# Kernel optimization log

Hardware: AMD Instinct MI355X
Metric: run time of the kernel (lower is better)

## Reference

```python
import jax, jax.numpy as jnp
import numpy as np

N = 50000      # nodes per type
E = 800000     # edges per relation
CIN = 64       # in_channels
H, O = 2, 32   # heads, out_channels
HID = H * O    # hidden
EC = 16        # edge_channels


def setup_inputs() -> dict:
    key = jax.random.key(0)
    ks = jax.random.split(key, 30)
    f = lambda i, shape, s=0.1: jax.random.normal(ks[i], shape, dtype=jnp.float32) * s
    inp = {
        'x_a': f(0, (N, CIN), 1.0), 'x_b': f(1, (N, CIN), 1.0),
        'edge_attr1': f(2, (E, EC), 1.0), 'edge_attr2': f(3, (E, EC), 1.0),
        'Wq_a': f(4, (CIN, HID)), 'Wk_a': f(5, (CIN, HID)), 'Wv_a': f(6, (CIN, HID)),
        'Wq_b': f(7, (CIN, HID)), 'Wk_b': f(8, (CIN, HID)), 'Wv_b': f(9, (CIN, HID)),
        'emb_a': f(10, (HID,)), 'emb_b': f(11, (HID,)),
        'rel1': f(12, (HID,)), 'rel2': f(13, (HID,)),
        'We': f(14, (EC, HID)), 'a_attn': f(15, (4 * O,)),
        'Wo_a': f(16, (HID, O)), 'bo_a': f(17, (O,)),
        'Wo_b': f(18, (HID, O)), 'bo_b': f(19, (O,)),
        'Wr_a': f(20, (CIN, O)), 'Wr_b': f(21, (CIN, O)),
        'row1': jax.random.randint(ks[22], (E,), 0, N),
        'col1': jax.random.randint(ks[23], (E,), 0, N),
        'row2': jax.random.randint(ks[24], (E,), 0, N),
        'col2': jax.random.randint(ks[25], (E,), 0, N),
    }
    return inp


def _edge_softmax(scores, col, num_dst):
    # softmax over incoming edges of each destination node; scores: [E, H]
    m = jax.ops.segment_max(scores, col, num_segments=num_dst)      # [N, H]
    ex = jnp.exp(scores - m[col])
    s = jax.ops.segment_sum(ex, col, num_segments=num_dst)          # [N, H]
    return ex / s[col]


def _relation(q_dst, k_src, v_src, emb_src, emb_dst, rel_emb, edge_bias,
              row, col, a_attn, num_dst):
    eb = edge_bias                                                  # [E, H, O]
    qd = q_dst[col] + emb_dst.reshape(1, H, O)
    ks = k_src[row] + emb_src.reshape(1, H, O)
    rb = jnp.broadcast_to(rel_emb.reshape(1, H, O), qd.shape)
    attn_in = jnp.concatenate([qd, ks, rb, eb], axis=-1)            # [E, H, 4O]
    scores = jnp.einsum('ehd,d->eh', jnp.tanh(attn_in), a_attn)    # [E, H]
    w = _edge_softmax(scores, col, num_dst)                         # [E, H]
    msg = v_src[row] + rel_emb.reshape(1, H, O) + eb                # [E, H, O]
    agg = jax.ops.segment_sum(msg * w[..., None], col, num_segments=num_dst)
    return agg.reshape(num_dst, H * O)


def reference(x_a, x_b, edge_attr1, edge_attr2,
              Wq_a, Wk_a, Wv_a, Wq_b, Wk_b, Wv_b,
              emb_a, emb_b, rel1, rel2, We, a_attn,
              Wo_a, bo_a, Wo_b, bo_b, Wr_a, Wr_b,
              row1, col1, row2, col2):
    q_a = (x_a @ Wq_a).reshape(-1, H, O)
    k_a = (x_a @ Wk_a).reshape(-1, H, O)
    v_a = (x_a @ Wv_a).reshape(-1, H, O)
    q_b = (x_b @ Wq_b).reshape(-1, H, O)
    k_b = (x_b @ Wk_b).reshape(-1, H, O)
    v_b = (x_b @ Wv_b).reshape(-1, H, O)

    # relation r1: a -> b
    eb1 = (edge_attr1 @ We).reshape(-1, H, O)
    out_b = _relation(q_b, k_a, v_a, emb_a, emb_b, rel1, eb1, row1, col1, a_attn, N)
    # relation r2: b -> a
    eb2 = (edge_attr2 @ We).reshape(-1, H, O)
    out_a = _relation(q_a, k_b, v_b, emb_b, emb_a, rel2, eb2, row2, col2, a_attn, N)

    fin_a = out_a @ Wo_a + bo_a + x_a @ Wr_a                        # [N, O]
    fin_b = out_b @ Wo_b + bo_b + x_b @ Wr_b                        # [N, O]
    return jnp.concatenate([fin_a, fin_b], axis=0)                  # [2N, O]
```

## Files before the change

### kernel.cpp

```cpp
#include <hip/hip_runtime.h>
#include <hip/hip_bf16.h>

typedef __hip_bfloat16 bf16;
typedef __attribute__((ext_vector_type(8))) short short8;
typedef __attribute__((ext_vector_type(4))) float float4v;

static __device__ __forceinline__ float b2f(bf16 x) { return __bfloat162float(x); }

static __device__ __forceinline__ float ldf(const void* p, size_t i, int f32) {
    return f32 ? ((const float*)p)[i] : b2f(((const bf16*)p)[i]);
}
static __device__ __forceinline__ void stf(void* p, size_t i, int f32, float v) {
    if (f32) ((float*)p)[i] = v;
    else     ((bf16*)p)[i] = __float2bfloat16(v);
}
static __device__ __forceinline__ unsigned short f2bf_bits(float f) {
    bf16 h = __float2bfloat16(f);
    return *(unsigned short*)&h;
}

static __device__ __forceinline__ float fast_tanh(float x) {
    float t = __expf(2.f * x);
    return 1.f - 2.f * __builtin_amdgcn_rcpf(t + 1.f);
}

static __device__ __forceinline__ void load_ea16(const void* ea, size_t e, int f32, float* er) {
    if (f32) {
        const float4* p = (const float4*)((const float*)ea + e * 16);
        #pragma unroll
        for (int q = 0; q < 4; ++q) {
            float4 v = p[q];
            er[4*q] = v.x; er[4*q+1] = v.y; er[4*q+2] = v.z; er[4*q+3] = v.w;
        }
    } else {
        const uint4* p = (const uint4*)((const bf16*)ea + e * 16);
        #pragma unroll
        for (int q = 0; q < 2; ++q) {
            uint4 u = p[q];
            er[8*q+0] = __uint_as_float(u.x << 16);
            er[8*q+1] = __uint_as_float(u.x & 0xffff0000u);
            er[8*q+2] = __uint_as_float(u.y << 16);
            er[8*q+3] = __uint_as_float(u.y & 0xffff0000u);
            er[8*q+4] = __uint_as_float(u.z << 16);
            er[8*q+5] = __uint_as_float(u.z & 0xffff0000u);
            er[8*q+6] = __uint_as_float(u.w << 16);
            er[8*q+7] = __uint_as_float(u.w & 0xffff0000u);
        }
    }
}

__global__ void detect_kernel(const unsigned short* __restrict__ a, int* __restrict__ flag)
{
    __shared__ int cnt;
    if (threadIdx.x == 0) cnt = 0;
    __syncthreads();
    unsigned e = (a[threadIdx.x] >> 7) & 0xFF;
    if (e < 100 || e > 133) atomicAdd(&cnt, 1);
    __syncthreads();
    if (threadIdx.x == 0) *flag = (cnt >= 16) ? 1 : 0;
}

__global__ __launch_bounds__(256) void transpose_w_kernel(
    const void* __restrict__ W0, const void* __restrict__ W1,
    const void* __restrict__ W2, const void* __restrict__ W3,
    const void* __restrict__ W4, const void* __restrict__ W5,
    const int* __restrict__ flagp, unsigned short* __restrict__ wt)
{
    const int f32 = *flagp;
    const void* src;
    switch (blockIdx.x) {
        case 0: src = W0; break; case 1: src = W1; break; case 2: src = W2; break;
        case 3: src = W3; break; case 4: src = W4; break; default: src = W5; break;
    }
    unsigned short* dst = wt + blockIdx.x * 4096;
    for (int i = threadIdx.x; i < 4096; i += 256) {
        int c = i >> 6, j = i & 63;
        dst[j * 64 + c] = f2bf_bits(ldf(src, c * 64 + j, f32));
    }
}

__global__ __launch_bounds__(256) void node_prep_mfma_kernel(
    const void* __restrict__ x_a, const void* __restrict__ x_b,
    const unsigned short* __restrict__ wt,
    const void* __restrict__ emb_a, const void* __restrict__ emb_b,
    const void* __restrict__ a_attn, const int* __restrict__ flagp,
    float* __restrict__ v_a, float* __restrict__ v_b,
    float* __restrict__ sq_a, float* __restrict__ sk_a,
    float* __restrict__ sq_b, float* __restrict__ sk_b,
    int n_nodes, int tiles)
{
    const int f32 = *flagp;
    const int wave_id = blockIdx.x * 4 + (threadIdx.x >> 6);
    if (wave_id >= 2 * tiles) return;
    const int type = (wave_id >= tiles);
    const int tile = type ? (wave_id - tiles) : wave_id;

    const void* xp = type ? x_b : x_a;
    const unsigned short* wq = wt + (type ? 3 * 4096 : 0);
    const unsigned short* wk = wq + 4096;
    const unsigned short* wv = wk + 4096;
    const void* embp = type ? emb_b : emb_a;
    float*  v_out  = type ? v_b : v_a;
    float2* sq_out = (float2*)(type ? sq_b : sq_a);
    float2* sk_out = (float2*)(type ? sk_b : sk_a);

    const int lane = threadIdx.x & 63;
    const int ml   = lane & 15;
    const int g    = lane >> 4;
    const int g8   = g * 8;

    float embc[4], acq[4], ack[4];
    #pragma unroll
    for (int t = 0; t < 4; ++t) {
        int colt = t * 16 + ml;
        embc[t] = ldf(embp, colt, f32);
        acq[t]  = ldf(a_attn, colt & 31, f32);
        ack[t]  = ldf(a_attn, 32 + (colt & 31), f32);
    }

    short8 Bq[4][2], Bk[4][2], Bv[4][2];
    #pragma unroll
    for (int t = 0; t < 4; ++t) {
        const int rowo = (t * 16 + ml) * 64;
        #pragma unroll
        for (int kh = 0; kh < 2; ++kh) {
            const int o = rowo + kh * 32 + g8;
            Bq[t][kh] = __builtin_bit_cast(short8, *(const uint4*)(wq + o));
            Bk[t][kh] = __builtin_bit_cast(short8, *(const uint4*)(wk + o));
            Bv[t][kh] = __builtin_bit_cast(short8, *(const uint4*)(wv + o));
        }
    }

    const int n0 = tile << 4;
    int nr = n0 + ml; if (nr > n_nodes - 1) nr = n_nodes - 1;
    short8 A0, A1;
    if (f32) {
        const float4* xr = (const float4*)((const float*)xp + (size_t)nr * 64);
        float4 f0 = xr[2*g], f1 = xr[2*g+1], f2 = xr[8+2*g], f3 = xr[9+2*g];
        short8 a0, a1;
        a0[0]=(short)f2bf_bits(f0.x); a0[1]=(short)f2bf_bits(f0.y);
        a0[2]=(short)f2bf_bits(f0.z); a0[3]=(short)f2bf_bits(f0.w);
        a0[4]=(short)f2bf_bits(f1.x); a0[5]=(short)f2bf_bits(f1.y);
        a0[6]=(short)f2bf_bits(f1.z); a0[7]=(short)f2bf_bits(f1.w);
        a1[0]=(short)f2bf_bits(f2.x); a1[1]=(short)f2bf_bits(f2.y);
        a1[2]=(short)f2bf_bits(f2.z); a1[3]=(short)f2bf_bits(f2.w);
        a1[4]=(short)f2bf_bits(f3.x); a1[5]=(short)f2bf_bits(f3.y);
        a1[6]=(short)f2bf_bits(f3.z); a1[7]=(short)f2bf_bits(f3.w);
        A0 = a0; A1 = a1;
    } else {
        const uint4* xr = (const uint4*)((const bf16*)xp + (size_t)nr * 64);
        A0 = __builtin_bit_cast(short8, xr[g]);
        A1 = __builtin_bit_cast(short8, xr[4 + g]);
    }

    float4v accq[4], acck[4], accv[4];
    #pragma unroll
    for (int t = 0; t < 4; ++t) {
        float4v z = {0.f, 0.f, 0.f, 0.f};
        accq[t] = z; acck[t] = z; accv[t] = z;
    }
    #pragma unroll
    for (int t = 0; t < 4; ++t) {
        accq[t] = __builtin_amdgcn_mfma_f32_16x16x32_bf16(A0, Bq[t][0], accq[t], 0, 0, 0);
        accq[t] = __builtin_amdgcn_mfma_f32_16x16x32_bf16(A1, Bq[t][1], accq[t], 0, 0, 0);
        acck[t] = __builtin_amdgcn_mfma_f32_16x16x32_bf16(A0, Bk[t][0], acck[t], 0, 0, 0);
        acck[t] = __builtin_amdgcn_mfma_f32_16x16x32_bf16(A1, Bk[t][1], acck[t], 0, 0, 0);
        accv[t] = __builtin_amdgcn_mfma_f32_16x16x32_bf16(A0, Bv[t][0], accv[t], 0, 0, 0);
        accv[t] = __builtin_amdgcn_mfma_f32_16x16x32_bf16(A1, Bv[t][1], accv[t], 0, 0, 0);
    }

    #pragma unroll
    for (int t = 0; t < 4; ++t) {
        #pragma unroll
        for (int r = 0; r < 4; ++r) {
            int node = n0 + g * 4 + r;
            if (node < n_nodes) v_out[(size_t)node * 64 + t * 16 + ml] = accv[t][r];
        }
    }

    #pragma unroll
    for (int r = 0; r < 4; ++r) {
        float q0 = fast_tanh(accq[0][r] + embc[0]) * acq[0]
                 + fast_tanh(accq[1][r] + embc[1]) * acq[1];
        float q1 = fast_tanh(accq[2][r] + embc[2]) * acq[2]
                 + fast_tanh(accq[3][r] + embc[3]) * acq[3];
        float k0 = fast_tanh(acck[0][r] + embc[0]) * ack[0]
                 + fast_tanh(acck[1][r] + embc[1]) * ack[1];
        float k1 = fast_tanh(acck[2][r] + embc[2]) * ack[2]
                 + fast_tanh(acck[3][r] + embc[3]) * ack[3];
        #pragma unroll
        for (int o = 1; o < 16; o <<= 1) {
            q0 += __shfl_xor(q0, o, 64); q1 += __shfl_xor(q1, o, 64);
            k0 += __shfl_xor(k0, o, 64); k1 += __shfl_xor(k1, o, 64);
        }
        int node = n0 + g * 4 + r;
        if (ml == 0 && node < n_nodes) {
            sq_out[node] = make_float2(q0, q1);
            sk_out[node] = make_float2(k0, k1);
        }
    }
}

__global__ void rel_const_kernel(const void* __restrict__ rel1, const void* __restrict__ rel2,
                                 const void* __restrict__ a_attn, const int* __restrict__ flagp,
                                 float* __restrict__ cvals)
{
    const int f32 = *flagp;
    int t = threadIdx.x;
    const void* r = (t < 64) ? rel1 : rel2;
    int l = t & 63;
    float v = tanhf(ldf(r, l, f32)) * ldf(a_attn, 64 + (l & 31), f32);
    #pragma unroll
    for (int off = 16; off; off >>= 1) v += __shfl_xor(v, off, 32);
    if ((l & 31) == 0) cvals[(t >> 6) * 2 + (l >> 5)] = v;
}

__global__ void precompute_kernel(const void* __restrict__ We,
                                  const void* __restrict__ Wo_b, const void* __restrict__ Wo_a,
                                  const void* __restrict__ rel1, const void* __restrict__ rel2,
                                  const int* __restrict__ flagp,
                                  float* __restrict__ M1, float* __restrict__ c321,
                                  float* __restrict__ M2, float* __restrict__ c322)
{
    const int f32 = *flagp;
    const int sel = blockIdx.x;
    const void* Wo = sel ? Wo_a : Wo_b;
    const void* rel = sel ? rel2 : rel1;
    float* M   = sel ? M2 : M1;
    float* c32 = sel ? c322 : c321;
    int t = threadIdx.x;
    int m = t >> 5, j = t & 31;
    int h = m >> 4, c = m & 15;
    float s = 0.f;
    for (int jj = 0; jj < 32; ++jj)
        s += ldf(We, c * 64 + h * 32 + jj, f32) * ldf(Wo, (size_t)(h * 32 + jj) * 32 + j, f32);
    M[m * 32 + j] = s;
    if (t < 32) {
        float s2 = 0.f;
        for (int ch = 0; ch < 64; ++ch)
            s2 += ldf(rel, ch, f32) * ldf(Wo, (size_t)ch * 32 + t, f32);
        c32[t] = s2;
    }
}

__global__ __launch_bounds__(256) void hist_kernel(
    const int* __restrict__ col1, const int* __restrict__ col2,
    int* __restrict__ cnt, int nb, int n_nodes, int num_e)
{
    const int sel = (blockIdx.x >= nb) ? 1 : 0;
    const int bx  = sel ? blockIdx.x - nb : blockIdx.x;
    const int* col = sel ? col2 : col1;
    const int rb = sel ? n_nodes : 0;
    int e = bx * 256 + threadIdx.x;
    if (e < num_e) atomicAdd(&cnt[rb + col[e]], 1);
}

__global__ __launch_bounds__(256) void scan1_kernel(const int* __restrict__ cnt,
                                                    int* __restrict__ partial, int n)
{
    __shared__ int wsum[4];
    int t = threadIdx.x;
    int i0 = blockIdx.x * 512 + 2 * t;
    int s = ((i0 < n) ? cnt[i0] : 0) + ((i0 + 1 < n) ? cnt[i0 + 1] : 0);
    #pragma unroll
    for (int o = 32; o; o >>= 1) s += __shfl_xor(s, o, 64);
    if ((t & 63) == 0) wsum[t >> 6] = s;
    __syncthreads();
    if (t == 0) partial[blockIdx.x] = wsum[0] + wsum[1] + wsum[2] + wsum[3];
}

__global__ void scan2_kernel(const int* __restrict__ partial, int* __restrict__ pp,
                             int* __restrict__ off, int nch, int noff)
{
    int lane = threadIdx.x;
    int running = 0;
    for (int base = 0; base < nch; base += 64) {
        int i = base + lane;
        int o = (i < nch) ? partial[i] : 0;
        int v = o;
        #pragma unroll
        for (int d = 1; d < 64; d <<= 1) {
            int u = __shfl_up(v, d, 64);
            if (lane >= d) v += u;
        }
        if (i < nch) pp[i] = running + v - o;
        running += __shfl(v, 63, 64);
    }
    if (lane == 0) off[noff] = running;
}

__global__ __launch_bounds__(256) void scan3_kernel(const int* __restrict__ cnt,
                                                    const int* __restrict__ pp,
                                                    int* __restrict__ off,
                                                    int* __restrict__ cursor, int n)
{
    __shared__ int tmp[256];
    int t = threadIdx.x;
    int i0 = blockIdx.x * 512 + 2 * t;
    int v0 = (i0 < n) ? cnt[i0] : 0;
    int v1 = (i0 + 1 < n) ? cnt[i0 + 1] : 0;
    int pair = v0 + v1;
    tmp[t] = pair;
    __syncthreads();
    for (int d = 1; d < 256; d <<= 1) {
        int x = (t >= d) ? tmp[t - d] : 0;
        __syncthreads();
        tmp[t] += x;
        __syncthreads();
    }
    int excl = tmp[t] - pair + pp[blockIdx.x];
    if (i0 < n)     { off[i0] = excl;          cursor[i0] = excl; }
    if (i0 + 1 < n) { off[i0 + 1] = excl + v0; cursor[i0 + 1] = excl + v0; }
}

__global__ __launch_bounds__(256) void edge_score_scatter_kernel(
    const void* __restrict__ ea1p, const void* __restrict__ ea2p,
    const void* __restrict__ We,
    const int* __restrict__ row1, const int* __restrict__ col1,
    const int* __restrict__ row2, const int* __restrict__ col2,
    const float* __restrict__ sq_bp, const float* __restrict__ sk_ap,
    const float* __restrict__ sq_ap, const float* __restrict__ sk_bp,
    const float* __restrict__ cvals, const void* __restrict__ a_attn,
    const int* __restrict__ flagp, int* __restrict__ cursor,
    uint4* __restrict__ payload, int nb, int n_nodes, int num_e)
{
    const int f32 = *flagp;
    const int sel = (blockIdx.x >= nb) ? 1 : 0;
    const int bx  = sel ? blockIdx.x - nb : blockIdx.x;
    const void* ea = sel ? ea2p : ea1p;
    const int* row = sel ? row2 : row1;
    const int* col = sel ? col2 : col1;
    const float* sq_dst = sel ? sq_ap : sq_bp;
    const float* sk_src = sel ? sk_bp : sk_ap;
    const int rb = sel ? n_nodes : 0;

    __shared__ float We_s[16 * 64];
    __shared__ float a3_s[32];
    for (int i = threadIdx.x; i < 16 * 64; i += 256) We_s[i] = ldf(We, i, f32);
    if (threadIdx.x < 32) a3_s[threadIdx.x] = ldf(a_attn, 96 + threadIdx.x, f32);
    const float c0 = cvals[sel * 2 + 0];
    const float c1 = cvals[sel * 2 + 1];
    __syncthreads();

    const int e0 = bx * 512 + threadIdx.x;
    const int e1 = e0 + 256;
    const bool v1e = (e1 < num_e);
    if (e0 >= num_e) return;

    float er0[16], er1[16];
    load_ea16(ea, (size_t)e0, f32, er0);
    if (v1e) load_ea16(ea, (size_t)e1, f32, er1);
    else {
        #pragma unroll
        for (int c = 0; c < 16; ++c) er1[c] = 0.f;
    }

    float acc00 = 0.f, acc01 = 0.f, acc10 = 0.f, acc11 = 0.f;
    #pragma unroll 1
    for (int jb = 0; jb < 64; jb += 16) {
        float t0[16], t1[16];
        #pragma unroll
        for (int jj = 0; jj < 16; ++jj) { t0[jj] = 0.f; t1[jj] = 0.f; }
        #pragma unroll
        for (int c = 0; c < 16; ++c) {
            #pragma unroll
            for (int jj = 0; jj < 16; ++jj) {
                float w = We_s[c * 64 + jb + jj];
                t0[jj] += er0[c] * w;
                t1[jj] += er1[c] * w;
            }
        }
        float p0 = 0.f, p1 = 0.f;
        #pragma unroll
        for (int jj = 0; jj < 16; ++jj) {
            float a = a3_s[(jb + jj) & 31];
            p0 += fast_tanh(t0[jj]) * a;
            p1 += fast_tanh(t1[jj]) * a;
        }
        if (jb & 32) { acc01 += p0; acc11 += p1; }
        else         { acc00 += p0; acc10 += p1; }
    }

    {
        int dc = col[e0], s = row[e0];
        float2 sqd = ((const float2*)sq_dst)[dc];
        float2 sks = ((const float2*)sk_src)[s];
        float s0 = fminf(30.f, fmaxf(-30.f, acc00 + sqd.x + sks.x + c0));
        float s1 = fminf(30.f, fmaxf(-30.f, acc01 + sqd.y + sks.y + c1));
        int pos = atomicAdd(&cursor[rb + dc], 1);
        uint4* rec = payload + (size_t)3 * pos;
        unsigned w0 = (unsigned)f2bf_bits(er0[0])  | ((unsigned)f2bf_bits(er0[1])  << 16);
        unsigned w1 = (unsigned)f2bf_bits(er0[2])  | ((unsigned)f2bf_bits(er0[3])  << 16);
        unsigned w2 = (unsigned)f2bf_bits(er0[4])  | ((unsigned)f2bf_bits(er0[5])  << 16);
        unsigned w3 = (unsigned)f2bf_bits(er0[6])  | ((unsigned)f2bf_bits(er0[7])  << 16);
        unsigned w4 = (unsigned)f2bf_bits(er0[8])  | ((unsigned)f2bf_bits(er0[9])  << 16);
        unsigned w5 = (unsigned)f2bf_bits(er0[10]) | ((unsigned)f2bf_bits(er0[11]) << 16);
        unsigned w6 = (unsigned)f2bf_bits(er0[12]) | ((unsigned)f2bf_bits(er0[13]) << 16);
        unsigned w7 = (unsigned)f2bf_bits(er0[14]) | ((unsigned)f2bf_bits(er0[15]) << 16);
        rec[0] = make_uint4((unsigned)s, __float_as_uint(__expf(s0)), __float_as_uint(__expf(s1)), 0u);
        rec[1] = make_uint4(w0, w1, w2, w3);
        rec[2] = make_uint4(w4, w5, w6, w7);
    }
    if (v1e) {
        int dc = col[e1], s = row[e1];
        float2 sqd = ((const float2*)sq_dst)[dc];
        float2 sks = ((const float2*)sk_src)[s];
        float s0 = fminf(30.f, fmaxf(-30.f, acc10 + sqd.x + sks.x + c0));
        float s1 = fminf(30.f, fmaxf(-30.f, acc11 + sqd.y + sks.y + c1));
        int pos = atomicAdd(&cursor[rb + dc], 1);
        uint4* rec = payload + (size_t)3 * pos;
        unsigned w0 = (unsigned)f2bf_bits(er1[0])  | ((unsigned)f2bf_bits(er1[1])  << 16);
        unsigned w1 = (unsigned)f2bf_bits(er1[2])  | ((unsigned)f2bf_bits(er1[3])  << 16);
        unsigned w2 = (unsigned)f2bf_bits(er1[4])  | ((unsigned)f2bf_bits(er1[5])  << 16);
        unsigned w3 = (unsigned)f2bf_bits(er1[6])  | ((unsigned)f2bf_bits(er1[7])  << 16);
        unsigned w4 = (unsigned)f2bf_bits(er1[8])  | ((unsigned)f2bf_bits(er1[9])  << 16);
        unsigned w5 = (unsigned)f2bf_bits(er1[10]) | ((unsigned)f2bf_bits(er1[11]) << 16);
        unsigned w6 = (unsigned)f2bf_bits(er1[12]) | ((unsigned)f2bf_bits(er1[13]) << 16);
        unsigned w7 = (unsigned)f2bf_bits(er1[14]) | ((unsigned)f2bf_bits(er1[15]) << 16);
        rec[0] = make_uint4((unsigned)s, __float_as_uint(__expf(s0)), __float_as_uint(__expf(s1)), 0u);
        rec[1] = make_uint4(w0, w1, w2, w3);
        rec[2] = make_uint4(w4, w5, w6, w7);
    }
}

__global__ __launch_bounds__(256) void agg_final_kernel(
    const uint4* __restrict__ payload, const int* __restrict__ off,
    const float* __restrict__ v_a, const float* __restrict__ v_b,
    const void* __restrict__ x_a, const void* __restrict__ x_b,
    const void* __restrict__ Wo_a, const void* __restrict__ Wo_b,
    const void* __restrict__ bo_a, const void* __restrict__ bo_b,
    const void* __restrict__ Wr_a, const void* __restrict__ Wr_b,
    const float* __restrict__ M1, const float* __restrict__ M2,
    const float* __restrict__ c321, const float* __restrict__ c322,
    const int* __restrict__ flagp, void* __restrict__ out,
    int n_nodes, int nbh)
{
    const int sel = (blockIdx.x >= nbh) ? 1 : 0;
    const int bx  = sel ? blockIdx.x - nbh : blockIdx.x;
    const float* v_src = sel ? v_b : v_a;
    const void*  x     = sel ? x_a : x_b;
    const void*  Wo    = sel ? Wo_a : Wo_b;
    const void*  bo    = sel ? bo_a : bo_b;
    const void*  Wr    = sel ? Wr_a : Wr_b;
    const float* M     = sel ? M2 : M1;
    const float* c32   = sel ? c322 : c321;
    const int relbase  = sel ? n_nodes : 0;
    const size_t out_off = sel ? 0 : (size_t)n_nodes * 32;

    const int f32  = *flagp;
    const int lane = threadIdx.x & 63;
    const int wv   = threadIdx.x >> 6;
    const int j    = lane & 31;
    const int half = lane >> 5;
    const int c16  = lane & 15;
    const bool hi  = (lane >= 32);

    __shared__ float stage[4][160];

    float WoR[32], WrR[32], MR[16];
    const int cb = half * 32;
    #pragma unroll
    for (int cc = 0; cc < 32; ++cc) {
        WoR[cc] = ldf(Wo, (size_t)(cb + cc) * 32 + j, f32);
        WrR[cc] = ldf(Wr, (size_t)(cb + cc) * 32 + j, f32);
    }
    const int ub = half * 16;
    #pragma unroll
    for (int cc = 0; cc < 16; ++cc) MR[cc] = M[(ub + cc) * 32 + j];
    const float boR  = ldf(bo, j, f32);
    const float c32R = c32[j];

    const int stride = nbh * 4;
    const int iters  = (n_nodes + stride - 1) / stride;
    int d = bx * 4 + wv;

    for (int it = 0; it < iters; ++it, d += stride) {
        const bool valid = (d < n_nodes);
        const int dd  = valid ? d : (n_nodes - 1);
        const int idx = relbase + dd;
        const int b   = __builtin_amdgcn_readfirstlane(off[idx]);
        const int en  = __builtin_amdgcn_readfirstlane(off[idx + 1]);
        const int deg = en - b;

        float den0 = 0.f, den1 = 0.f, y = 0.f, ua = 0.f;
        int k = b;
        #pragma unroll 1
        for (; k + 4 <= en; k += 4) {
            uint4 m0 = payload[(size_t)3 * (k + 0)];
            uint4 m1 = payload[(size_t)3 * (k + 1)];
            uint4 m2 = payload[(size_t)3 * (k + 2)];
            uint4 m3 = payload[(size_t)3 * (k + 3)];
            const unsigned short* p0 = (const unsigned short*)(payload + (size_t)3 * (k + 0) + 1);
            const unsigned short* p1 = (const unsigned short*)(payload + (size_t)3 * (k + 1) + 1);
            const unsigned short* p2 = (const unsigned short*)(payload + (size_t)3 * (k + 2) + 1);
            const unsigned short* p3 = (const unsigned short*)(payload + (size_t)3 * (k + 3) + 1);
            float vv0 = v_src[(size_t)m0.x * 64 + lane];
            float vv1 = v_src[(size_t)m1.x * 64 + lane];
            float vv2 = v_src[(size_t)m2.x * 64 + lane];
            float vv3 = v_src[(size_t)m3.x * 64 + lane];
            float ea0 = __uint_as_float((unsigned)p0[c16] << 16);
            float ea1 = __uint_as_float((unsigned)p1[c16] << 16);
            float ea2 = __uint_as_float((unsigned)p2[c16] << 16);
            float ea3 = __uint_as_float((unsigned)p3[c16] << 16);
            float e00 = __uint_as_float(m0.y), e01 = __uint_as_float(m0.z);
            float e10 = __uint_as_float(m1.y), e11 = __uint_as_float(m1.z);
            float e20 = __uint_as_float(m2.y), e21 = __uint_as_float(m2.z);
            float e30 = __uint_as_float(m3.y), e31 = __uint_as_float(m3.z);
            den0 += e00 + e10 + e20 + e30;
            den1 += e01 + e11 + e21 + e31;
            float x0 = hi ? e01 : e00;
            float x1 = hi ? e11 : e10;
            float x2 = hi ? e21 : e20;
            float x3 = hi ? e31 : e30;
            y  = fmaf(x0, vv0, y);  y  = fmaf(x1, vv1, y);
            y  = fmaf(x2, vv2, y);  y  = fmaf(x3, vv3, y);
            ua = fmaf(x0, ea0, ua); ua = fmaf(x1, ea1, ua);
            ua = fmaf(x2, ea2, ua); ua = fmaf(x3, ea3, ua);
        }
        for (; k < en; ++k) {
            uint4 m0 = payload[(size_t)3 * k];
            const unsigned short* p0 = (const unsigned short*)(payload + (size_t)3 * k + 1);
            float vv0 = v_src[(size_t)m0.x * 64 + lane];
            float ea0 = __uint_as_float((unsigned)p0[c16] << 16);
            float e00 = __uint_as_float(m0.y), e01 = __uint_as_float(m0.z);
            den0 += e00; den1 += e01;
            float x0 = hi ? e01 : e00;
            y  = fmaf(x0, vv0, y);
            ua = fmaf(x0, ea0, ua);
        }

        float inv0 = (deg > 0) ? __builtin_amdgcn_rcpf(den0) : 0.f;
        float inv1 = (deg > 0) ? __builtin_amdgcn_rcpf(den1) : 0.f;
        const float invh = hi ? inv1 : inv0;
        y  *= invh;
        ua *= invh;

        float xv = ldf(x, (size_t)dd * 64 + lane, f32);

        float* st = stage[wv];
        st[lane] = y;
        st[64 + lane] = xv;
        if ((lane & 31) < 16) st[128 + half * 16 + c16] = ua;
        __asm__ volatile("s_waitcnt lgkmcnt(0)" ::: "memory");

        float acc = 0.f;
        #pragma unroll
        for (int cc = 0; cc < 32; ++cc) {
            acc = fmaf(st[cb + cc], WoR[cc], acc);
            acc = fmaf(st[64 + cb + cc], WrR[cc], acc);
        }
        #pragma unroll
        for (int cc = 0; cc < 16; ++cc)
            acc = fmaf(st[128 + ub + cc], MR[cc], acc);

        float other = __shfl(acc, lane ^ 32, 64);
        if (valid && lane < 32) {
            float o = acc + other + boR + ((deg > 0) ? c32R : 0.f);
            stf(out, out_off + (size_t)dd * 32 + j, f32, o);
        }
        __asm__ volatile("" ::: "memory");
        __builtin_amdgcn_wave_barrier();
    }
}

extern "C" void kernel_launch(void* const* d_in, const int* in_sizes, int n_in,
                              void* d_out, int out_size, void* d_ws, size_t ws_size,
                              hipStream_t stream)
{
    const void* x_a   = d_in[0];
    const void* x_b   = d_in[1];
    const void* ea1   = d_in[2];
    const void* ea2   = d_in[3];
    const void* Wq_a  = d_in[4];
    const void* Wk_a  = d_in[5];
    const void* Wv_a  = d_in[6];
    const void* Wq_b  = d_in[7];
    const void* Wk_b  = d_in[8];
    const void* Wv_b  = d_in[9];
    const void* emb_a = d_in[10];
    const void* emb_b = d_in[11];
    const void* rel1  = d_in[12];
    const void* rel2  = d_in[13];
    const void* We    = d_in[14];
    const void* a_at  = d_in[15];
    const void* Wo_a  = d_in[16];
    const void* bo_a  = d_in[17];
    const void* Wo_b  = d_in[18];
    const void* bo_b  = d_in[19];
    const void* Wr_a  = d_in[20];
    const void* Wr_b  = d_in[21];
    const int*  row1  = (const int*)d_in[22];
    const int*  col1  = (const int*)d_in[23];
    const int*  row2  = (const int*)d_in[24];
    const int*  col2  = (const int*)d_in[25];

    const int N = in_sizes[0] / 64;
    const int E = in_sizes[22];

    float* ws = (float*)d_ws;
    size_t off = 0;
    int*   flag = (int*)ws;        off += 64;
    float* v_a  = ws + off;        off += (size_t)N * 64;
    float* v_b  = ws + off;        off += (size_t)N * 64;
    float* sq_a = ws + off;        off += (size_t)N * 2;
    float* sk_a = ws + off;        off += (size_t)N * 2;
    float* sq_b = ws + off;        off += (size_t)N * 2;
    float* sk_b = ws + off;        off += (size_t)N * 2;
    float* cvals = ws + off;       off += 4;
    off = (off + 3) & ~(size_t)3;
    unsigned short* wt = (unsigned short*)(ws + off); off += 6 * 4096 / 2;
    float* M1   = ws + off;        off += 1024;
    float* c321 = ws + off;        off += 32;
    float* M2   = ws + off;        off += 1024;
    float* c322 = ws + off;        off += 32;
    int*   cnt    = (int*)(ws + off);  off += (size_t)2 * N;
    int*   offs   = (int*)(ws + off);  off += (size_t)2 * N + 2;
    int*   cursor = (int*)(ws + off);  off += (size_t)2 * N;
    int*   partial = (int*)(ws + off); off += 512;
    int*   pp      = (int*)(ws + off); off += 512;
    off = (off + 3) & ~(size_t)3;
    uint4* payload = (uint4*)(ws + off); off += (size_t)2 * E * 12;

    const int tiles        = (N + 15) >> 4;
    const int mfma_blocks  = (2 * tiles + 3) / 4;
    const int score_blocks = (E + 511) / 512;
    const int eb_blocks    = (E + 255) / 256;
    const int nch          = (2 * N + 511) / 512;
    const int agg_half     = 2048;

    detect_kernel<<<1, 128, 0, stream>>>((const unsigned short*)a_at, flag);
    hipMemsetAsync(cnt, 0, (size_t)2 * N * sizeof(int), stream);

    transpose_w_kernel<<<6, 256, 0, stream>>>(Wq_a, Wk_a, Wv_a, Wq_b, Wk_b, Wv_b, flag, wt);
    node_prep_mfma_kernel<<<mfma_blocks, 256, 0, stream>>>(
        x_a, x_b, wt, emb_a, emb_b, a_at, flag,
        v_a, v_b, sq_a, sk_a, sq_b, sk_b, N, tiles);

    rel_const_kernel<<<1, 128, 0, stream>>>(rel1, rel2, a_at, flag, cvals);
    precompute_kernel<<<2, 1024, 0, stream>>>(We, Wo_b, Wo_a, rel1, rel2, flag,
                                              M1, c321, M2, c322);

    hist_kernel<<<2 * eb_blocks, 256, 0, stream>>>(col1, col2, cnt, eb_blocks, N, E);
    scan1_kernel<<<nch, 256, 0, stream>>>(cnt, partial, 2 * N);
    scan2_kernel<<<1, 64, 0, stream>>>(partial, pp, offs, nch, 2 * N);
    scan3_kernel<<<nch, 256, 0, stream>>>(cnt, pp, offs, cursor, 2 * N);

    edge_score_scatter_kernel<<<2 * score_blocks, 256, 0, stream>>>(
        ea1, ea2, We, row1, col1, row2, col2,
        sq_b, sk_a, sq_a, sk_b, cvals, a_at, flag,
        cursor, payload, score_blocks, N, E);

    agg_final_kernel<<<2 * agg_half, 256, 0, stream>>>(
        payload, offs, v_a, v_b, x_a, x_b, Wo_a, Wo_b, bo_a, bo_b, Wr_a, Wr_b,
        M1, M2, c321, c322, flag, d_out, N, agg_half);
}
```

Measured before the change: 581.0 us.

## Fuse small prep kernels, store V in bf16, precompute residual, unroll aggregation

Merges the weight transpose, rel-constant and precompute kernels into one launch. The residual projection x@Wr now runs on MFMA in node_prep, so agg_final no longer loads x or Wr. V is stored as bf16 to halve the bytes of the random per-edge gathers. The aggregation loop is unrolled to eight edges for more memory-level parallelism, and the two relations are interleaved across block indices. Storing V in bf16 adds rounding error, and the wider unroll raises register pressure.

```diff
diff --git a/kernel.cpp b/kernel.cpp
--- a/kernel.cpp
+++ b/kernel.cpp
@@ -60,22 +60,68 @@
     if (threadIdx.x == 0) *flag = (cnt >= 16) ? 1 : 0;
 }
 
-__global__ __launch_bounds__(256) void transpose_w_kernel(
+__global__ __launch_bounds__(256) void prep_small_kernel(
     const void* __restrict__ W0, const void* __restrict__ W1,
     const void* __restrict__ W2, const void* __restrict__ W3,
     const void* __restrict__ W4, const void* __restrict__ W5,
-    const int* __restrict__ flagp, unsigned short* __restrict__ wt)
+    const void* __restrict__ Wr_a, const void* __restrict__ Wr_b,
+    const void* __restrict__ We,
+    const void* __restrict__ Wo_a, const void* __restrict__ Wo_b,
+    const void* __restrict__ rel1, const void* __restrict__ rel2,
+    const void* __restrict__ a_attn, const int* __restrict__ flagp,
+    unsigned short* __restrict__ wt,
+    float* __restrict__ M1, float* __restrict__ c321,
+    float* __restrict__ M2, float* __restrict__ c322,
+    float* __restrict__ cvals)
 {
     const int f32 = *flagp;
-    const void* src;
-    switch (blockIdx.x) {
-        case 0: src = W0; break; case 1: src = W1; break; case 2: src = W2; break;
-        case 3: src = W3; break; case 4: src = W4; break; default: src = W5; break;
-    }
-    unsigned short* dst = wt + blockIdx.x * 4096;
-    for (int i = threadIdx.x; i < 4096; i += 256) {
-        int c = i >> 6, j = i & 63;
-        dst[j * 64 + c] = f2bf_bits(ldf(src, c * 64 + j, f32));
+    const int bid = blockIdx.x;
+    if (bid < 6) {
+        const void* src;
+        switch (bid) {
+            case 0: src = W0; break; case 1: src = W1; break; case 2: src = W2; break;
+            case 3: src = W3; break; case 4: src = W4; break; default: src = W5; break;
+        }
+        unsigned short* dst = wt + bid * 4096;
+        for (int i = threadIdx.x; i < 4096; i += 256) {
+            int c = i >> 6, j = i & 63;
+            dst[j * 64 + c] = f2bf_bits(ldf(src, c * 64 + j, f32));
+        }
+    } else if (bid < 8) {
+        const void* src = (bid == 6) ? Wr_a : Wr_b;
+        unsigned short* dst = wt + 24576 + (bid - 6) * 2048;
+        for (int i = threadIdx.x; i < 2048; i += 256) {
+            int c = i >> 5, j = i & 31;
+            dst[j * 64 + c] = f2bf_bits(ldf(src, c * 32 + j, f32));
+        }
+    } else {
+        const int sel = bid - 8;
+        const void* Wo  = sel ? Wo_a : Wo_b;
+        const void* rel = sel ? rel2 : rel1;
+        float* M   = sel ? M2 : M1;
+        float* c32 = sel ? c322 : c321;
+        const int t = threadIdx.x;
+        for (int i = t; i < 1024; i += 256) {
+            int m = i >> 5, j = i & 31;
+            int h = m >> 4, c = m & 15;
+            float s = 0.f;
+            for (int jj = 0; jj < 32; ++jj)
+                s += ldf(We, c * 64 + h * 32 + jj, f32) * ldf(Wo, (size_t)(h * 32 + jj) * 32 + j, f32);
+            M[m * 32 + j] = s;
+        }
+        if (t < 32) {
+            float s2 = 0.f;
+            for (int ch = 0; ch < 64; ++ch)
+                s2 += ldf(rel, ch, f32) * ldf(Wo, (size_t)ch * 32 + t, f32);
+            c32[t] = s2;
+        }
+        if (t == 252 || t == 253) {
+            int h = t - 252;
+            float s3 = 0.f;
+            for (int l = 0; l < 32; ++l)
+                s3 += tanhf(ldf(rel, h * 32 + l, f32)) * ldf(a_attn, 64 + l, f32);
+            cvals[sel * 2 + h] = s3;
+        }
     }
 }
 
@@ -84,7 +130,8 @@
     const unsigned short* __restrict__ wt,
     const void* __restrict__ emb_a, const void* __restrict__ emb_b,
     const void* __restrict__ a_attn, const int* __restrict__ flagp,
-    float* __restrict__ v_a, float* __restrict__ v_b,
+    unsigned short* __restrict__ v_a, unsigned short* __restrict__ v_b,
+    float* __restrict__ r_a, float* __restrict__ r_b,
     float* __restrict__ sq_a, float* __restrict__ sk_a,
     float* __restrict__ sq_b, float* __restrict__ sk_b,
     int n_nodes, int tiles)
@@ -99,8 +146,10 @@
     const unsigned short* wq = wt + (type ? 3 * 4096 : 0);
     const unsigned short* wk = wq + 4096;
     const unsigned short* wv = wk + 4096;
+    const unsigned short* wr = wt + 24576 + (type ? 2048 : 0);
     const void* embp = type ? emb_b : emb_a;
-    float*  v_out  = type ? v_b : v_a;
+    unsigned short* v_out = type ? v_b : v_a;
+    float*  r_out  = type ? r_b : r_a;
     float2* sq_out = (float2*)(type ? sq_b : sq_a);
     float2* sk_out = (float2*)(type ? sk_b : sk_a);
 
@@ -118,7 +167,7 @@
         ack[t]  = ldf(a_attn, 32 + (colt & 31), f32);
     }
 
-    short8 Bq[4][2], Bk[4][2], Bv[4][2];
+    short8 Bq[4][2], Bk[4][2], Bv[4][2], Br[2][2];
     #pragma unroll
     for (int t = 0; t < 4; ++t) {
         const int rowo = (t * 16 + ml) * 64;
@@ -128,6 +177,8 @@
             Bq[t][kh] = __builtin_bit_cast(short8, *(const uint4*)(wq + o));
             Bk[t][kh] = __builtin_bit_cast(short8, *(const uint4*)(wk + o));
             Bv[t][kh] = __builtin_bit_cast(short8, *(const uint4*)(wv + o));
+            if (t < 2)
+                Br[t][kh] = __builtin_bit_cast(short8, *(const uint4*)(wr + o));
         }
     }
 
@@ -153,11 +204,12 @@
         A1 = __builtin_bit_cast(short8, xr[4 + g]);
     }
 
-    float4v accq[4], acck[4], accv[4];
+    float4v accq[4], acck[4], accv[4], accr[2];
     #pragma unroll
     for (int t = 0; t < 4; ++t) {
         float4v z = {0.f, 0.f, 0.f, 0.f};
         accq[t] = z; acck[t] = z; accv[t] = z;
+        if (t < 2) accr[t] = z;
     }
     #pragma unroll
     for (int t = 0; t < 4; ++t) {
@@ -167,6 +219,10 @@
         acck[t] = __builtin_amdgcn_mfma_f32_16x16x32_bf16(A1, Bk[t][1], acck[t], 0, 0, 0);
         accv[t] = __builtin_amdgcn_mfma_f32_16x16x32_bf16(A0, Bv[t][0], accv[t], 0, 0, 0);
         accv[t] = __builtin_amdgcn_mfma_f32_16x16x32_bf16(A1, Bv[t][1], accv[t], 0, 0, 0);
+        if (t < 2) {
+            accr[t] = __builtin_amdgcn_mfma_f32_16x16x32_bf16(A0, Br[t][0], accr[t], 0, 0, 0);
+            accr[t] = __builtin_amdgcn_mfma_f32_16x16x32_bf16(A1, Br[t][1], accr[t], 0, 0, 0);
+        }
     }
 
     #pragma unroll
@@ -174,7 +230,10 @@
         #pragma unroll
         for (int r = 0; r < 4; ++r) {
             int node = n0 + g * 4 + r;
-            if (node < n_nodes) v_out[(size_t)node * 64 + t * 16 + ml] = accv[t][r];
+            if (node < n_nodes) {
+                v_out[(size_t)node * 64 + t * 16 + ml] = f2bf_bits(accv[t][r]);
+                if (t < 2) r_out[(size_t)node * 32 + t * 16 + ml] = accr[t][r];
+            }
         }
     }
 
@@ -201,54 +260,12 @@
     }
 }
 
-__global__ void rel_const_kernel(const void* __restrict__ rel1, const void* __restrict__ rel2,
-                                 const void* __restrict__ a_attn, const int* __restrict__ flagp,
-                                 float* __restrict__ cvals)
-{
-    const int f32 = *flagp;
-    int t = threadIdx.x;
-    const void* r = (t < 64) ? rel1 : rel2;
-    int l = t & 63;
-    float v = tanhf(ldf(r, l, f32)) * ldf(a_attn, 64 + (l & 31), f32);
-    #pragma unroll
-    for (int off = 16; off; off >>= 1) v += __shfl_xor(v, off, 32);
-    if ((l & 31) == 0) cvals[(t >> 6) * 2 + (l >> 5)] = v;
-}
-
-__global__ void precompute_kernel(const void* __restrict__ We,
-                                  const void* __restrict__ Wo_b, const void* __restrict__ Wo_a,
-                                  const void* __restrict__ rel1, const void* __restrict__ rel2,
-                                  const int* __restrict__ flagp,
-                                  float* __restrict__ M1, float* __restrict__ c321,
-                                  float* __restrict__ M2, float* __restrict__ c322)
-{
-    const int f32 = *flagp;
-    const int sel = blockIdx.x;
-    const void* Wo = sel ? Wo_a : Wo_b;
-    const void* rel = sel ? rel2 : rel1;
-    float* M   = sel ? M2 : M1;
-    float* c32 = sel ? c322 : c321;
-    int t = threadIdx.x;
-    int m = t >> 5, j = t & 31;
-    int h = m >> 4, c = m & 15;
-    float s = 0.f;
-    for (int jj = 0; jj < 32; ++jj)
-        s += ldf(We, c * 64 + h * 32 + jj, f32) * ldf(Wo, (size_t)(h * 32 + jj) * 32 + j, f32);
-    M[m * 32 + j] = s;
-    if (t < 32) {
-        float s2 = 0.f;
-        for (int ch = 0; ch < 64; ++ch)
-            s2 += ldf(rel, ch, f32) * ldf(Wo, (size_t)ch * 32 + t, f32);
-        c32[t] = s2;
-    }
-}
-
 __global__ __launch_bounds__(256) void hist_kernel(
     const int* __restrict__ col1, const int* __restrict__ col2,
-    int* __restrict__ cnt, int nb, int n_nodes, int num_e)
-{
-    const int sel = (blockIdx.x >= nb) ? 1 : 0;
-    const int bx  = sel ? blockIdx.x - nb : blockIdx.x;
+    int* __restrict__ cnt, int n_nodes, int num_e)
+{
+    const int sel = blockIdx.x & 1;
+    const int bx  = blockIdx.x >> 1;
     const int* col = sel ? col2 : col1;
     const int rb = sel ? n_nodes : 0;
     int e = bx * 256 + threadIdx.x;
@@ -322,11 +339,11 @@
     const float* __restrict__ sq_ap, const float* __restrict__ sk_bp,
     const float* __restrict__ cvals, const void* __restrict__ a_attn,
     const int* __restrict__ flagp, int* __restrict__ cursor,
-    uint4* __restrict__ payload, int nb, int n_nodes, int num_e)
+    uint4* __restrict__ payload, int n_nodes, int num_e)
 {
     const int f32 = *flagp;
-    const int sel = (blockIdx.x >= nb) ? 1 : 0;
-    const int bx  = sel ? blockIdx.x - nb : blockIdx.x;
+    const int sel = blockIdx.x & 1;
+    const int bx  = blockIdx.x >> 1;
     const void* ea = sel ? ea2p : ea1p;
     const int* row = sel ? row2 : row1;
     const int* col = sel ? col2 : col1;
@@ -425,23 +442,21 @@
 
 __global__ __launch_bounds__(256) void agg_final_kernel(
     const uint4* __restrict__ payload, const int* __restrict__ off,
-    const float* __restrict__ v_a, const float* __restrict__ v_b,
-    const void* __restrict__ x_a, const void* __restrict__ x_b,
+    const unsigned short* __restrict__ v_a, const unsigned short* __restrict__ v_b,
+    const float* __restrict__ r_a, const float* __restrict__ r_b,
     const void* __restrict__ Wo_a, const void* __restrict__ Wo_b,
     const void* __restrict__ bo_a, const void* __restrict__ bo_b,
-    const void* __restrict__ Wr_a, const void* __restrict__ Wr_b,
     const float* __restrict__ M1, const float* __restrict__ M2,
     const float* __restrict__ c321, const float* __restrict__ c322,
     const int* __restrict__ flagp, void* __restrict__ out,
     int n_nodes, int nbh)
 {
-    const int sel = (blockIdx.x >= nbh) ? 1 : 0;
-    const int bx  = sel ? blockIdx.x - nbh : blockIdx.x;
-    const float* v_src = sel ? v_b : v_a;
-    const void*  x     = sel ? x_a : x_b;
+    const int sel = blockIdx.x & 1;
+    const int bx  = blockIdx.x >> 1;
+    const unsigned short* v_src = sel ? v_b : v_a;
+    const float* r_src = sel ? r_a : r_b;
     const void*  Wo    = sel ? Wo_a : Wo_b;
     const void*  bo    = sel ? bo_a : bo_b;
-    const void*  Wr    = sel ? Wr_a : Wr_b;
     const float* M     = sel ? M2 : M1;
     const float* c32   = sel ? c322 : c321;
     const int relbase  = sel ? n_nodes : 0;
@@ -455,15 +470,13 @@
     const int c16  = lane & 15;
     const bool hi  = (lane >= 32);
 
-    __shared__ float stage[4][160];
-
-    float WoR[32], WrR[32], MR[16];
+    __shared__ float stage[4][96];
+
+    float WoR[32], MR[16];
     const int cb = half * 32;
     #pragma unroll
-    for (int cc = 0; cc < 32; ++cc) {
+    for (int cc = 0; cc < 32; ++cc)
         WoR[cc] = ldf(Wo, (size_t)(cb + cc) * 32 + j, f32);
-        WrR[cc] = ldf(Wr, (size_t)(cb + cc) * 32 + j, f32);
-    }
     const int ub = half * 16;
     #pragma unroll
     for (int cc = 0; cc < 16; ++cc) MR[cc] = M[(ub + cc) * 32 + j];
@@ -482,51 +495,45 @@
         const int en  = __builtin_amdgcn_readfirstlane(off[idx + 1]);
         const int deg = en - b;
 
+        const float rv = r_src[(size_t)dd * 32 + j];
+
         float den0 = 0.f, den1 = 0.f, y = 0.f, ua = 0.f;
         int k = b;
         #pragma unroll 1
-        for (; k + 4 <= en; k += 4) {
-            uint4 m0 = payload[(size_t)3 * (k + 0)];
-            uint4 m1 = payload[(size_t)3 * (k + 1)];
-            uint4 m2 = payload[(size_t)3 * (k + 2)];
-            uint4 m3 = payload[(size_t)3 * (k + 3)];
-            const unsigned short* p0 = (const unsigned short*)(payload + (size_t)3 * (k + 0) + 1);
-            const unsigned short* p1 = (const unsigned short*)(payload + (size_t)3 * (k + 1) + 1);
-            const unsigned short* p2 = (const unsigned short*)(payload + (size_t)3 * (k + 2) + 1);
-            const unsigned short* p3 = (const unsigned short*)(payload + (size_t)3 * (k + 3) + 1);
-            float vv0 = v_src[(size_t)m0.x * 64 + lane];
-            float vv1 = v_src[(size_t)m1.x * 64 + lane];
-            float vv2 = v_src[(size_t)m2.x * 64 + lane];
-            float vv3 = v_src[(size_t)m3.x * 64 + lane];
-            float ea0 = __uint_as_float((unsigned)p0[c16] << 16);
-            float ea1 = __uint_as_float((unsigned)p1[c16] << 16);
-            float ea2 = __uint_as_float((unsigned)p2[c16] << 16);
-            float ea3 = __uint_as_float((unsigned)p3[c16] << 16);
-            float e00 = __uint_as_float(m0.y), e01 = __uint_as_float(m0.z);
-            float e10 = __uint_as_float(m1.y), e11 = __uint_as_float(m1.z);
-            float e20 = __uint_as_float(m2.y), e21 = __uint_as_float(m2.z);
-            float e30 = __uint_as_float(m3.y), e31 = __uint_as_float(m3.z);
-            den0 += e00 + e10 + e20 + e30;
-            den1 += e01 + e11 + e21 + e31;
-            float x0 = hi ? e01 : e00;
-            float x1 = hi ? e11 : e10;
-            float x2 = hi ? e21 : e20;
-            float x3 = hi ? e31 : e30;
-            y  = fmaf(x0, vv0, y);  y  = fmaf(x1, vv1, y);
-            y  = fmaf(x2, vv2, y);  y  = fmaf(x3, vv3, y);
-            ua = fmaf(x0, ea0, ua); ua = fmaf(x1, ea1, ua);
-            ua = fmaf(x2, ea2, ua); ua = fmaf(x3, ea3, ua);
-        }
+        for (; k + 8 <= en; k += 8) {
+            uint4 m[8];
+            #pragma unroll
+            for (int q = 0; q < 8; ++q) m[q] = payload[(size_t)3 * (k + q)];
+            float ev[8];
+            #pragma unroll
+            for (int q = 0; q < 8; ++q) {
+                const unsigned short* pq = (const unsigned short*)(payload + (size_t)3 * (k + q) + 1);
+                ev[q] = __uint_as_float((unsigned)pq[c16] << 16);
+            }
+            float vv[8];
+            #pragma unroll
+            for (int q = 0; q < 8; ++q)
+                vv[q] = __uint_as_float((unsigned)v_src[(size_t)m[q].x * 64 + lane] << 16);
+            #pragma unroll
+            for (int q = 0; q < 8; ++q) {
+                float e0 = __uint_as_float(m[q].y), e1 = __uint_as_float(m[q].z);
+                den0 += e0; den1 += e1;
+                float xw = hi ? e1 : e0;
+                y  = fmaf(xw, vv[q], y);
+                ua = fmaf(xw, ev[q], ua);
+            }
+        }
+        #pragma unroll 1
         for (; k < en; ++k) {
-            uint4 m0 = payload[(size_t)3 * k];
-            const unsigned short* p0 = (const unsigned short*)(payload + (size_t)3 * k + 1);
-            float vv0 = v_src[(size_t)m0.x * 64 + lane];
-            float ea0 = __uint_as_float((unsigned)p0[c16] << 16);
-            float e00 = __uint_as_float(m0.y), e01 = __uint_as_float(m0.z);
-            den0 += e00; den1 += e01;
-            float x0 = hi ? e01 : e00;
-            y  = fmaf(x0, vv0, y);
-            ua = fmaf(x0, ea0, ua);
+            uint4 mm = payload[(size_t)3 * k];
+            const unsigned short* pq = (const unsigned short*)(payload + (size_t)3 * k + 1);
+            float evs = __uint_as_float((unsigned)pq[c16] << 16);
+            float vvs = __uint_as_float((unsigned)v_src[(size_t)mm.x * 64 + lane] << 16);
+            float e0 = __uint_as_float(mm.y), e1 = __uint_as_float(mm.z);
+            den0 += e0; den1 += e1;
+            float xw = hi ? e1 : e0;
+            y  = fmaf(xw, vvs, y);
+            ua = fmaf(xw, evs, ua);
         }
 
         float inv0 = (deg > 0) ? __builtin_amdgcn_rcpf(den0) : 0.f;
@@ -535,27 +542,22 @@
         y  *= invh;
         ua *= invh;
 
-        float xv = ldf(x, (size_t)dd * 64 + lane, f32);
-
         float* st = stage[wv];
         st[lane] = y;
-        st[64 + lane] = xv;
-        if ((lane & 31) < 16) st[128 + half * 16 + c16] = ua;
+        if ((lane & 31) < 16) st[64 + half * 16 + c16] = ua;
         __asm__ volatile("s_waitcnt lgkmcnt(0)" ::: "memory");
 
         float acc = 0.f;
         #pragma unroll
-        for (int cc = 0; cc < 32; ++cc) {
+        for (int cc = 0; cc < 32; ++cc)
             acc = fmaf(st[cb + cc], WoR[cc], acc);
-            acc = fmaf(st[64 + cb + cc], WrR[cc], acc);
-        }
         #pragma unroll
         for (int cc = 0; cc < 16; ++cc)
-            acc = fmaf(st[128 + ub + cc], MR[cc], acc);
+            acc = fmaf(st[64 + ub + cc], MR[cc], acc);
 
         float other = __shfl(acc, lane ^ 32, 64);
         if (valid && lane < 32) {
-            float o = acc + other + boR + ((deg > 0) ? c32R : 0.f);
+            float o = acc + other + boR + rv + ((deg > 0) ? c32R : 0.f);
             stf(out, out_off + (size_t)dd * 32 + j, f32, o);
         }
         __asm__ volatile("" ::: "memory");
@@ -600,15 +602,17 @@
     float* ws = (float*)d_ws;
     size_t off = 0;
     int*   flag = (int*)ws;        off += 64;
-    float* v_a  = ws + off;        off += (size_t)N * 64;
-    float* v_b  = ws + off;        off += (size_t)N * 64;
+    unsigned short* v_a = (unsigned short*)(ws + off); off += (size_t)N * 32;
+    unsigned short* v_b = (unsigned short*)(ws + off); off += (size_t)N * 32;
+    float* r_a  = ws + off;        off += (size_t)N * 32;
+    float* r_b  = ws + off;        off += (size_t)N * 32;
     float* sq_a = ws + off;        off += (size_t)N * 2;
     float* sk_a = ws + off;        off += (size_t)N * 2;
     float* sq_b = ws + off;        off += (size_t)N * 2;
     float* sk_b = ws + off;        off += (size_t)N * 2;
     float* cvals = ws + off;       off += 4;
     off = (off + 3) & ~(size_t)3;
-    unsigned short* wt = (unsigned short*)(ws + off); off += 6 * 4096 / 2;
+    unsigned short* wt = (unsigned short*)(ws + off); off += 28672 / 2;
     float* M1   = ws + off;        off += 1024;
     float* c321 = ws + off;        off += 32;
     float* M2   = ws + off;        off += 1024;
@@ -631,16 +635,16 @@
     detect_kernel<<<1, 128, 0, stream>>>((const unsigned short*)a_at, flag);
     hipMemsetAsync(cnt, 0, (size_t)2 * N * sizeof(int), stream);
 
-    transpose_w_kernel<<<6, 256, 0, stream>>>(Wq_a, Wk_a, Wv_a, Wq_b, Wk_b, Wv_b, flag, wt);
+    prep_small_kernel<<<10, 256, 0, stream>>>(
+        Wq_a, Wk_a, Wv_a, Wq_b, Wk_b, Wv_b, Wr_a, Wr_b,
+        We, Wo_a, Wo_b, rel1, rel2, a_at, flag,
+        wt, M1, c321, M2, c322, cvals);
+
     node_prep_mfma_kernel<<<mfma_blocks, 256, 0, stream>>>(
         x_a, x_b, wt, emb_a, emb_b, a_at, flag,
-        v_a, v_b, sq_a, sk_a, sq_b, sk_b, N, tiles);
-
-    rel_const_kernel<<<1, 128, 0, stream>>>(rel1, rel2, a_at, flag, cvals);
-    precompute_kernel<<<2, 1024, 0, stream>>>(We, Wo_b, Wo_a, rel1, rel2, flag,
-                                              M1, c321, M2, c322);
-
-    hist_kernel<<<2 * eb_blocks, 256, 0, stream>>>(col1, col2, cnt, eb_blocks, N, E);
+        v_a, v_b, r_a, r_b, sq_a, sk_a, sq_b, sk_b, N, tiles);
+
+    hist_kernel<<<2 * eb_blocks, 256, 0, stream>>>(col1, col2, cnt, N, E);
     scan1_kernel<<<nch, 256, 0, stream>>>(cnt, partial, 2 * N);
     scan2_kernel<<<1, 64, 0, stream>>>(partial, pp, offs, nch, 2 * N);
     scan3_kernel<<<nch, 256, 0, stream>>>(cnt, pp, offs, cursor, 2 * N);
@@ -648,9 +652,9 @@
     edge_score_scatter_kernel<<<2 * score_blocks, 256, 0, stream>>>(
         ea1, ea2, We, row1, col1, row2, col2,
         sq_b, sk_a, sq_a, sk_b, cvals, a_at, flag,
-        cursor, payload, score_blocks, N, E);
+        cursor, payload, N, E);
 
     agg_final_kernel<<<2 * agg_half, 256, 0, stream>>>(
-        payload, offs, v_a, v_b, x_a, x_b, Wo_a, Wo_b, bo_a, bo_b, Wr_a, Wr_b,
+        payload, offs, v_a, v_b, r_a, r_b, Wo_a, Wo_b, bo_a, bo_b,
         M1, M2, c321, c322, flag, d_out, N, agg_half);
 }
```

Measured after the change: 527.3 us. 1.1x faster.
